# Kernel tuning notes

Hardware: AMD Instinct MI355X
Metric: run time of the kernel (lower is better)

The kernel has to match this reference:

```python
import jax, jax.numpy as jnp
import numpy as np

K = 7  # kernel_size (odd)
PAD = K // 2
EPS = 1e-12  # F.normalize eps


def setup_inputs() -> dict:
    key = jax.random.key(0)
    kx, ky = jax.random.split(key)
    B, C, H, W = 4, 256, 256, 256
    x = jax.random.normal(kx, (B, C, H, W), dtype=jnp.float32)
    y = jax.random.normal(ky, (B, C, H, W), dtype=jnp.float32)
    return {"x": x, "y": y}


def _l2_normalize(t):
    # F.normalize(t, p=2, dim=1): divide by channel L2 norm, clamped at eps
    n = jnp.sqrt(jnp.sum(t * t, axis=1, keepdims=True))
    return t / jnp.maximum(n, EPS)


def reference(x, y):
    xn = _l2_normalize(x)
    yn = _l2_normalize(y)
    B, C, H, W = x.shape  # H == W assumed (module mixes h/w in slicing)
    yp = jnp.pad(yn, ((0, 0), (0, 0), (PAD, PAD), (PAD, PAD)))
    # Fixed K*K offset loop (small, static); each term reduces over channels.
    sims = [
        jnp.sum(xn * jax.lax.dynamic_slice(yp, (0, 0, i, j), (B, C, H, W)), axis=1)
        for i in range(K)
        for j in range(K)
    ]
    return jnp.stack(sims, axis=1)  # [B, K*K, H, W]
```

## Files before the change

kernel.cpp:

```cpp
#include <hip/hip_runtime.h>


#define H_ 256
#define W_ 256
#define C_ 256
#define B_ 4
#define TH 16
#define TW 16
#define KCH 32
#define NCHUNK (C_ / KCH)
#define HAL (TH + 6)
#define WAL (TW + 6)
#define YW 32
#define PLANE (H_ * W_)

typedef __attribute__((ext_vector_type(8))) short short8;
typedef __attribute__((ext_vector_type(4))) float floatx4;

__device__ __forceinline__ unsigned bfpair(float a, float b) {
  unsigned ua = __float_as_uint(a), ub = __float_as_uint(b);
  ua = (ua + 0x7FFFu + ((ua >> 16) & 1u)) >> 16;
  ub = (ub + 0x7FFFu + ((ub >> 16) & 1u)) & 0xFFFF0000u;
  return ub | ua;
}

__global__ __launch_bounds__(1024) void ncorr(const float* __restrict__ x,
                                              const float* __restrict__ y,
                                              float* __restrict__ out) {
  __shared__ short Yb[HAL * YW * KCH];
  __shared__ short Xb[TH * TW * KCH];
  __shared__ float sxl[TH * TW];
  __shared__ float syl[HAL * WAL];

  const int t = threadIdx.x;
  const int b = blockIdx.z;
  const int h0 = blockIdx.y * TH;
  const int w0 = blockIdx.x * TW;

  for (int idx = t; idx < HAL * 10 * (KCH / 2); idx += 1024) {
    int hy = idx / (10 * (KCH / 2));
    int r = idx - hy * (10 * (KCH / 2));
    int wy = 22 + r / (KCH / 2);
    int cp = r - (r / (KCH / 2)) * (KCH / 2);
    ((unsigned*)Yb)[((hy * YW + wy) * KCH) / 2 + cp] = 0u;
  }
  if (t < TH * TW) sxl[t] = 0.f;
  if (t < HAL * WAL) syl[t] = 0.f;

  int xidx[4], xlds[4];
  float sxacc[4];
#pragma unroll
  for (int i = 0; i < 4; i++) {
    int s = t + i * 1024;
    int cp = s >> 8;
    int h = (s >> 4) & 15;
    int w = s & 15;
    xidx[i] = ((b * C_ + 2 * cp) * H_ + (h0 + h)) * W_ + (w0 + w);
    xlds[i] = (h * TW + w) * KCH + 2 * cp;
    sxacc[i] = 0.f;
  }
  int yidx[8], ylds[8], ysl[8];
  float syacc[8];
  unsigned yok = 0;
#pragma unroll
  for (int i = 0; i < 8; i++) {
    int s = t + i * 1024;
    int cp = s / 484;
    int r = s - cp * 484;
    int hy = r / 22;
    int wy = r - hy * 22;
    int gy = h0 - 3 + hy;
    int gx = w0 - 3 + wy;
    bool inimg = (gy >= 0) && (gy < H_) && (gx >= 0) && (gx < W_);
    if (inimg) yok |= (1u << i);
    yidx[i] = ((b * C_ + 2 * cp) * H_ + (inimg ? gy : 0)) * W_ + (inimg ? gx : 0);
    ylds[i] = (hy * YW + wy) * KCH + 2 * cp;
    ysl[i] = r;
    syacc[i] = 0.f;
  }

  const int lane = t & 63;
  const int wv = t >> 6;
  const int q = lane >> 4;
  const int lr = lane & 15;

  floatx4 acc[7][2];
#pragma unroll
  for (int i = 0; i < 7; i++) {
    acc[i][0] = (floatx4){0.f, 0.f, 0.f, 0.f};
    acc[i][1] = (floatx4){0.f, 0.f, 0.f, 0.f};
  }

  for (int ch = 0; ch < NCHUNK; ch++) {
    __syncthreads();
    const int coff = ch * (KCH * PLANE);
#pragma unroll
    for (int i = 0; i < 4; i++) {
      const float* p = x + xidx[i] + coff;
      float f0 = p[0], f1 = p[PLANE];
      sxacc[i] += f0 * f0 + f1 * f1;
      *(unsigned*)&Xb[xlds[i]] = bfpair(f0, f1);
    }
#pragma unroll
    for (int i = 0; i < 8; i++) {
      if (i == 7 && t >= 576) break;
      float f0 = 0.f, f1 = 0.f;
      if ((yok >> i) & 1) {
        const float* p = y + yidx[i] + coff;
        f0 = p[0];
        f1 = p[PLANE];
      }
      syacc[i] += f0 * f0 + f1 * f1;
      *(unsigned*)&Yb[ylds[i]] = bfpair(f0, f1);
    }
    __syncthreads();
    short8 A = *(const short8*)&Xb[(wv * TW + lr) * KCH + q * 8];
#pragma unroll
    for (int i = 0; i < 7; i++) {
      const int hy = wv + i;
#pragma unroll
      for (int nt = 0; nt < 2; nt++) {
        short8 Bf = *(const short8*)&Yb[(hy * YW + nt * 16 + lr) * KCH + q * 8];
        acc[i][nt] = __builtin_amdgcn_mfma_f32_16x16x32_bf16(A, Bf, acc[i][nt], 0, 0, 0);
      }
    }
  }

  __syncthreads();
#pragma unroll
  for (int i = 0; i < 4; i++) atomicAdd(&sxl[(t + i * 1024) & 255], sxacc[i]);
#pragma unroll
  for (int i = 0; i < 8; i++) {
    if (i == 7 && t >= 576) break;
    atomicAdd(&syl[ysl[i]], syacc[i]);
  }
  __syncthreads();
  if (t < TH * TW) sxl[t] = 1.f / fmaxf(sqrtf(sxl[t]), 1e-12f);
  if (t < HAL * WAL) syl[t] = 1.f / fmaxf(sqrtf(syl[t]), 1e-12f);
  __syncthreads();

  const int h = wv;
#pragma unroll
  for (int i = 0; i < 7; i++) {
#pragma unroll
    for (int nt = 0; nt < 2; nt++) {
      const int n = nt * 16 + lr;
#pragma unroll
      for (int r = 0; r < 4; r++) {
        const int m = q * 4 + r;
        const int j = n - m;
        if (j >= 0 && j < 7) {
          float v = acc[i][nt][r] * sxl[h * TW + m] * syl[(h + i) * WAL + n];
          out[((b * 49 + 7 * i + j) * H_ + (h0 + h)) * W_ + (w0 + m)] = v;
        }
      }
    }
  }
}

extern "C" void kernel_launch(void* const* d_in, const int* in_sizes, int n_in,
                              void* d_out, int out_size, void* d_ws, size_t ws_size,
                              hipStream_t stream) {
  const float* x = (const float*)d_in[0];
  const float* y = (const float*)d_in[1];
  float* out = (float*)d_out;
  dim3 grid(W_ / TW, H_ / TH, B_);
  ncorr<<<grid, 1024, 0, stream>>>(x, y, out);
}
```

Baseline: 826.6 us.

## Double-buffer Y in LDS, load X directly into MFMA registers, stage output

Reworks the main loop so the next chunk's x and y values are prefetched into registers while the current chunk's MFMAs run. Y goes into a double-buffered LDS layout, so only one barrier per chunk is needed. The X tile no longer passes through LDS: each lane loads its 8 channels straight into the A operand. The x norm is reduced with wave shuffles instead of LDS atomics. The block index is swizzled, and results are staged in LDS so they can be written back with coalesced nontemporal stores. In exchange, register pressure goes up, and the output staging buffer reuses the Y LDS space.

```diff
diff --git a/kernel.cpp b/kernel.cpp
--- a/kernel.cpp
+++ b/kernel.cpp
@@ -11,11 +11,11 @@
 #define NCHUNK (C_ / KCH)
 #define HAL (TH + 6)
 #define WAL (TW + 6)
-#define YW 32
 #define PLANE (H_ * W_)
 
 typedef __attribute__((ext_vector_type(8))) short short8;
 typedef __attribute__((ext_vector_type(4))) float floatx4;
+typedef __attribute__((ext_vector_type(4))) unsigned uint32x4;
 
 __device__ __forceinline__ unsigned bfpair(float a, float b) {
   unsigned ua = __float_as_uint(a), ub = __float_as_uint(b);
@@ -27,62 +27,43 @@
 __global__ __launch_bounds__(1024) void ncorr(const float* __restrict__ x,
                                               const float* __restrict__ y,
                                               float* __restrict__ out) {
-  __shared__ short Yb[HAL * YW * KCH];
-  __shared__ short Xb[TH * TW * KCH];
+  __shared__ __align__(16) short Yb[2][HAL * 4 * WAL * 8];
   __shared__ float sxl[TH * TW];
   __shared__ float syl[HAL * WAL];
+  float* Ob = (float*)&Yb[0][0];
 
   const int t = threadIdx.x;
-  const int b = blockIdx.z;
-  const int h0 = blockIdx.y * TH;
-  const int w0 = blockIdx.x * TW;
 
-  for (int idx = t; idx < HAL * 10 * (KCH / 2); idx += 1024) {
-    int hy = idx / (10 * (KCH / 2));
-    int r = idx - hy * (10 * (KCH / 2));
-    int wy = 22 + r / (KCH / 2);
-    int cp = r - (r / (KCH / 2)) * (KCH / 2);
-    ((unsigned*)Yb)[((hy * YW + wy) * KCH) / 2 + cp] = 0u;
-  }
-  if (t < TH * TW) sxl[t] = 0.f;
+  int id = (blockIdx.z * gridDim.y + blockIdx.y) * gridDim.x + blockIdx.x;
+  int sw = (id & 7) * 128 + (id >> 3);
+  const int b = sw >> 8;
+  const int h0 = ((sw >> 4) & 15) * TH;
+  const int w0 = (sw & 15) * TW;
+
   if (t < HAL * WAL) syl[t] = 0.f;
-
-  int xidx[4], xlds[4];
-  float sxacc[4];
-#pragma unroll
-  for (int i = 0; i < 4; i++) {
-    int s = t + i * 1024;
-    int cp = s >> 8;
-    int h = (s >> 4) & 15;
-    int w = s & 15;
-    xidx[i] = ((b * C_ + 2 * cp) * H_ + (h0 + h)) * W_ + (w0 + w);
-    xlds[i] = (h * TW + w) * KCH + 2 * cp;
-    sxacc[i] = 0.f;
-  }
-  int yidx[8], ylds[8], ysl[8];
-  float syacc[8];
-  unsigned yok = 0;
-#pragma unroll
-  for (int i = 0; i < 8; i++) {
-    int s = t + i * 1024;
-    int cp = s / 484;
-    int r = s - cp * 484;
-    int hy = r / 22;
-    int wy = r - hy * 22;
-    int gy = h0 - 3 + hy;
-    int gx = w0 - 3 + wy;
-    bool inimg = (gy >= 0) && (gy < H_) && (gx >= 0) && (gx < W_);
-    if (inimg) yok |= (1u << i);
-    yidx[i] = ((b * C_ + 2 * cp) * H_ + (inimg ? gy : 0)) * W_ + (inimg ? gx : 0);
-    ylds[i] = (hy * YW + wy) * KCH + 2 * cp;
-    ysl[i] = r;
-    syacc[i] = 0.f;
-  }
 
   const int lane = t & 63;
   const int wv = t >> 6;
   const int q = lane >> 4;
   const int lr = lane & 15;
+
+  const int xbase = ((b * C_ + q * 8) * H_ + (h0 + wv)) * W_ + (w0 + lr);
+
+  const bool yact = (t < 968);
+  bool yin = false;
+  int ybase = 0, yslot = 0, ypos = 0;
+  if (yact) {
+    int cg2 = t / 484;
+    int r = t - cg2 * 484;
+    int hy = r / 22;
+    int wy = r - hy * 22;
+    int gy = h0 - 3 + hy, gx = w0 - 3 + wy;
+    yin = (gy >= 0) && (gy < H_) && (gx >= 0) && (gx < W_);
+    ybase = ((b * C_ + cg2 * 16) * H_ + (yin ? gy : 0)) * W_ + (yin ? gx : 0);
+    yslot = (hy * 4 + cg2 * 2) * 22 + wy;
+    ypos = hy * 22 + wy;
+  }
+  float sxacc = 0.f, syacc = 0.f;
 
   floatx4 acc[7][2];
 #pragma unroll
@@ -91,55 +72,88 @@
     acc[i][1] = (floatx4){0.f, 0.f, 0.f, 0.f};
   }
 
+  const int w2a = lr;
+  const int w2b = (lr < 6) ? (16 + lr) : 21;
+
+  float xr[2][8];
+  float yr[2][16];
+#pragma unroll
+  for (int s = 0; s < 2; s++) {
+#pragma unroll
+    for (int k = 0; k < 16; k++) yr[s][k] = 0.f;
+  }
+
+#pragma unroll
+  for (int j = 0; j < 8; j++) xr[0][j] = x[xbase + j * PLANE];
+  if (yact) {
+    if (yin) {
+#pragma unroll
+      for (int k = 0; k < 16; k++) yr[0][k] = y[ybase + k * PLANE];
+    }
+    unsigned p[8];
+#pragma unroll
+    for (int k = 0; k < 8; k++) {
+      syacc += yr[0][2 * k] * yr[0][2 * k] + yr[0][2 * k + 1] * yr[0][2 * k + 1];
+      p[k] = bfpair(yr[0][2 * k], yr[0][2 * k + 1]);
+    }
+    uint32x4 v0 = {p[0], p[1], p[2], p[3]};
+    uint32x4 v1 = {p[4], p[5], p[6], p[7]};
+    *(uint32x4*)&Yb[0][yslot * 8] = v0;
+    *(uint32x4*)&Yb[0][(yslot + 22) * 8] = v1;
+  }
+  __syncthreads();
+
+#pragma unroll
   for (int ch = 0; ch < NCHUNK; ch++) {
-    __syncthreads();
-    const int coff = ch * (KCH * PLANE);
+    const int cur = ch & 1, nxt = cur ^ 1;
+    const int cof = (ch + 1) * KCH * PLANE;
+    if (ch < NCHUNK - 1) {
 #pragma unroll
-    for (int i = 0; i < 4; i++) {
-      const float* p = x + xidx[i] + coff;
-      float f0 = p[0], f1 = p[PLANE];
-      sxacc[i] += f0 * f0 + f1 * f1;
-      *(unsigned*)&Xb[xlds[i]] = bfpair(f0, f1);
+      for (int j = 0; j < 8; j++) xr[nxt][j] = x[xbase + cof + j * PLANE];
+      if (yact && yin) {
+#pragma unroll
+        for (int k = 0; k < 16; k++) yr[nxt][k] = y[ybase + cof + k * PLANE];
+      }
     }
+    uint32x4 av;
 #pragma unroll
-    for (int i = 0; i < 8; i++) {
-      if (i == 7 && t >= 576) break;
-      float f0 = 0.f, f1 = 0.f;
-      if ((yok >> i) & 1) {
-        const float* p = y + yidx[i] + coff;
-        f0 = p[0];
-        f1 = p[PLANE];
+    for (int k = 0; k < 4; k++) {
+      sxacc += xr[cur][2 * k] * xr[cur][2 * k] + xr[cur][2 * k + 1] * xr[cur][2 * k + 1];
+      av[k] = bfpair(xr[cur][2 * k], xr[cur][2 * k + 1]);
+    }
+    short8 A = __builtin_bit_cast(short8, av);
+#pragma unroll
+    for (int i = 0; i < 7; i++) {
+      const int rb = ((wv + i) * 4 + q) * 22;
+      short8 B0 = *(const short8*)&Yb[cur][(rb + w2a) * 8];
+      acc[i][0] = __builtin_amdgcn_mfma_f32_16x16x32_bf16(A, B0, acc[i][0], 0, 0, 0);
+      short8 B1 = *(const short8*)&Yb[cur][(rb + w2b) * 8];
+      acc[i][1] = __builtin_amdgcn_mfma_f32_16x16x32_bf16(A, B1, acc[i][1], 0, 0, 0);
+    }
+    if (ch < NCHUNK - 1 && yact) {
+      unsigned p[8];
+#pragma unroll
+      for (int k = 0; k < 8; k++) {
+        syacc += yr[nxt][2 * k] * yr[nxt][2 * k] + yr[nxt][2 * k + 1] * yr[nxt][2 * k + 1];
+        p[k] = bfpair(yr[nxt][2 * k], yr[nxt][2 * k + 1]);
       }
-      syacc[i] += f0 * f0 + f1 * f1;
-      *(unsigned*)&Yb[ylds[i]] = bfpair(f0, f1);
+      uint32x4 v0 = {p[0], p[1], p[2], p[3]};
+      uint32x4 v1 = {p[4], p[5], p[6], p[7]};
+      *(uint32x4*)&Yb[nxt][yslot * 8] = v0;
+      *(uint32x4*)&Yb[nxt][(yslot + 22) * 8] = v1;
     }
     __syncthreads();
-    short8 A = *(const short8*)&Xb[(wv * TW + lr) * KCH + q * 8];
-#pragma unroll
-    for (int i = 0; i < 7; i++) {
-      const int hy = wv + i;
-#pragma unroll
-      for (int nt = 0; nt < 2; nt++) {
-        short8 Bf = *(const short8*)&Yb[(hy * YW + nt * 16 + lr) * KCH + q * 8];
-        acc[i][nt] = __builtin_amdgcn_mfma_f32_16x16x32_bf16(A, Bf, acc[i][nt], 0, 0, 0);
-      }
-    }
   }
 
+  float xs = sxacc;
+  xs += __shfl_xor(xs, 16);
+  xs += __shfl_xor(xs, 32);
+  if (q == 0) sxl[wv * 16 + lr] = 1.f / fmaxf(sqrtf(xs), 1e-12f);
+  if (yact) atomicAdd(&syl[ypos], syacc);
   __syncthreads();
-#pragma unroll
-  for (int i = 0; i < 4; i++) atomicAdd(&sxl[(t + i * 1024) & 255], sxacc[i]);
-#pragma unroll
-  for (int i = 0; i < 8; i++) {
-    if (i == 7 && t >= 576) break;
-    atomicAdd(&syl[ysl[i]], syacc[i]);
-  }
-  __syncthreads();
-  if (t < TH * TW) sxl[t] = 1.f / fmaxf(sqrtf(sxl[t]), 1e-12f);
   if (t < HAL * WAL) syl[t] = 1.f / fmaxf(sqrtf(syl[t]), 1e-12f);
   __syncthreads();
 
-  const int h = wv;
 #pragma unroll
   for (int i = 0; i < 7; i++) {
 #pragma unroll
@@ -150,11 +164,19 @@
         const int m = q * 4 + r;
         const int j = n - m;
         if (j >= 0 && j < 7) {
-          float v = acc[i][nt][r] * sxl[h * TW + m] * syl[(h + i) * WAL + n];
-          out[((b * 49 + 7 * i + j) * H_ + (h0 + h)) * W_ + (w0 + m)] = v;
+          float v = acc[i][nt][r] * sxl[wv * 16 + m] * syl[(wv + i) * 22 + n];
+          Ob[(7 * i + j) * 260 + wv * 16 + m] = v;
         }
       }
     }
+  }
+  __syncthreads();
+  for (int idx = t; idx < 49 * 256; idx += 1024) {
+    const int chn = idx >> 8;
+    const int rem = idx & 255;
+    __builtin_nontemporal_store(
+        Ob[chn * 260 + rem],
+        &out[((b * 49 + chn) * H_ + h0 + (rem >> 4)) * W_ + (w0 + (rem & 15))]);
   }
 }
 
```

Result: faster. 741.1 us (-10.3%).
